# Kernel tuning notes

Hardware: AMD Instinct MI355X
Metric: run time of the kernel (lower is better)

## Reference

```python
import jax, jax.numpy as jnp
import numpy as np

RANK = 192      # wbits=4 -> rank 192 in prepare_grouped_lora
QMAX = 15.0     # 2**4 - 1 for 4-bit asymmetric quantization
EPS = 1e-8

def _fake_quant_weight(w):
    # Per-output-channel asymmetric min-max fake quantization (4-bit).
    wmin = jnp.minimum(w.min(axis=1, keepdims=True), 0.0)
    wmax = jnp.maximum(w.max(axis=1, keepdims=True), 0.0)
    scale = jnp.maximum((wmax - wmin) / QMAX, EPS)
    zero = jnp.round(-wmin / scale)
    q = jnp.clip(jnp.round(w / scale) + zero, 0.0, QMAX)
    return (q - zero) * scale

def setup_inputs() -> dict:
    key = jax.random.key(0)
    k1, k2, k3, k4, k5 = jax.random.split(key, 5)
    B, S, IN, OUT = 4, 2048, 4096, 11008
    x = jax.random.normal(k1, (B, S, IN), dtype=jnp.float32)
    weight = jax.random.normal(k2, (OUT, IN), dtype=jnp.float32) * 0.02
    Bd = jax.random.normal(k3, (OUT, RANK), dtype=jnp.float32) * 0.01
    Bu = jax.random.normal(k4, (RANK, IN), dtype=jnp.float32) * 0.01
    bias = jax.random.normal(k5, (OUT,), dtype=jnp.float32) * 0.01
    return {"x": x, "weight": weight, "Bd": Bd, "Bu": Bu, "bias": bias}

def reference(x, weight, Bd, Bu, bias):
    # LoRA delta: Bd[:, :rank] @ Bu[:rank, :]  (rank=192 for 4-bit)
    delta = jnp.einsum('or,ri->oi', Bd[:, :RANK], Bu[:RANK, :])
    w = _fake_quant_weight(weight + delta)          # [out, in]
    out = jnp.einsum('bsi,oi->bso', x, w) + bias    # F.linear
    return out
```

## Files before the change

kernel.cpp:

```cpp
#include <hip/hip_runtime.h>
#include <stdint.h>

#define M_ROWS 8192
#define N_OUT  11008
#define K_IN   4096
#define RANK   192

typedef __attribute__((ext_vector_type(8))) short bf16x8;
typedef __attribute__((ext_vector_type(4))) float f32x4;

#define GLDS16(g, l) __builtin_amdgcn_global_load_lds( \
    (const __attribute__((address_space(1))) unsigned int*)(g), \
    (__attribute__((address_space(3))) unsigned int*)(l), 16, 0, 0)

static __device__ __forceinline__ unsigned short f2bf(float f) {
    union { float f; unsigned int u; } a; a.f = f;
    unsigned int u = a.u;
    u += 0x7fffu + ((u >> 16) & 1u);
    return (unsigned short)(u >> 16);
}

__global__ __launch_bounds__(256) void k_delta_minmax(
    const float* __restrict__ Wg, const float* __restrict__ Bd,
    const float* __restrict__ Bu, float* __restrict__ wq,
    float* __restrict__ pmin, float* __restrict__ pmax)
{
    __shared__ float bdT[RANK][68];
    __shared__ float buS[8][256];
    const int t  = threadIdx.x;
    const int tx = t & 31, ty = t >> 5;
    const int row0 = blockIdx.x * 64;
    const int col0 = blockIdx.y * 256;

    for (int i = t; i < 64 * RANK; i += 256) {
        int r = i / RANK, k = i - r * RANK;
        bdT[k][r] = Bd[(size_t)(row0 + r) * RANK + k];
    }

    float acc[8][8];
#pragma unroll
    for (int a = 0; a < 8; ++a)
#pragma unroll
        for (int b = 0; b < 8; ++b) acc[a][b] = 0.0f;

    for (int kc = 0; kc < RANK / 8; ++kc) {
        __syncthreads();
#pragma unroll
        for (int j = 0; j < 8; ++j)
            buS[j][t] = Bu[(size_t)(kc * 8 + j) * K_IN + col0 + t];
        __syncthreads();
#pragma unroll
        for (int k = 0; k < 8; ++k) {
            float bd[8], bu[8];
#pragma unroll
            for (int rr = 0; rr < 8; ++rr) bd[rr] = bdT[kc * 8 + k][ty * 8 + rr];
#pragma unroll
            for (int cc = 0; cc < 8; ++cc) bu[cc] = buS[k][tx + 32 * cc];
#pragma unroll
            for (int rr = 0; rr < 8; ++rr)
#pragma unroll
                for (int cc = 0; cc < 8; ++cc)
                    acc[rr][cc] = fmaf(bd[rr], bu[cc], acc[rr][cc]);
        }
    }

    float rmin[8], rmax[8];
#pragma unroll
    for (int rr = 0; rr < 8; ++rr) { rmin[rr] = 3.0e38f; rmax[rr] = -3.0e38f; }
#pragma unroll
    for (int rr = 0; rr < 8; ++rr) {
        size_t gr = (size_t)(row0 + ty * 8 + rr);
#pragma unroll
        for (int cc = 0; cc < 8; ++cc) {
            size_t gc = (size_t)(col0 + tx + 32 * cc);
            float w = Wg[gr * K_IN + gc] + acc[rr][cc];
            wq[gr * K_IN + gc] = w;
            rmin[rr] = fminf(rmin[rr], w);
            rmax[rr] = fmaxf(rmax[rr], w);
        }
    }
#pragma unroll
    for (int off = 16; off >= 1; off >>= 1) {
#pragma unroll
        for (int rr = 0; rr < 8; ++rr) {
            rmin[rr] = fminf(rmin[rr], __shfl_xor(rmin[rr], off, 64));
            rmax[rr] = fmaxf(rmax[rr], __shfl_xor(rmax[rr], off, 64));
        }
    }
    if (tx == 0) {
#pragma unroll
        for (int rr = 0; rr < 8; ++rr) {
            int gr = row0 + ty * 8 + rr;
            pmin[(size_t)gr * 16 + blockIdx.y] = rmin[rr];
            pmax[(size_t)gr * 16 + blockIdx.y] = rmax[rr];
        }
    }
}

__global__ __launch_bounds__(256) void k_scale_zero(
    const float* __restrict__ pmin, const float* __restrict__ pmax,
    float* __restrict__ scale, float* __restrict__ zero)
{
    int r = blockIdx.x * 256 + threadIdx.x;
    if (r >= N_OUT) return;
    float mn = 0.0f, mx = 0.0f;
#pragma unroll
    for (int i = 0; i < 16; ++i) {
        mn = fminf(mn, pmin[(size_t)r * 16 + i]);
        mx = fmaxf(mx, pmax[(size_t)r * 16 + i]);
    }
    float s = fmaxf((mx - mn) / 15.0f, 1e-8f);
    scale[r] = s;
    zero[r] = rintf(-mn / s);
}

__global__ __launch_bounds__(256) void k_quant_cast(
    const float* __restrict__ wq, const float* __restrict__ scale,
    const float* __restrict__ zero, unsigned short* __restrict__ wb)
{
    size_t i = ((size_t)blockIdx.x * 256 + threadIdx.x) * 4;
    int r = (int)(i >> 12);
    float s = scale[r], z = zero[r];
    float4 v = *(const float4*)(wq + i);
    float in[4] = {v.x, v.y, v.z, v.w};
    unsigned short h[4];
#pragma unroll
    for (int j = 0; j < 4; ++j) {
        float q = rintf(in[j] / s) + z;
        q = fminf(fmaxf(q, 0.0f), 15.0f);
        h[j] = f2bf((q - z) * s);
    }
    unsigned int lo = (unsigned int)h[0] | ((unsigned int)h[1] << 16);
    unsigned int hi = (unsigned int)h[2] | ((unsigned int)h[3] << 16);
    *(unsigned long long*)(wb + i) = ((unsigned long long)hi << 32) | lo;
}

__global__ __launch_bounds__(256) void k_cast_x(
    const float* __restrict__ x, unsigned short* __restrict__ xb)
{
    size_t i = ((size_t)blockIdx.x * 256 + threadIdx.x) * 4;
    float4 v = *(const float4*)(x + i);
    unsigned int lo = (unsigned int)f2bf(v.x) | ((unsigned int)f2bf(v.y) << 16);
    unsigned int hi = (unsigned int)f2bf(v.z) | ((unsigned int)f2bf(v.w) << 16);
    *(unsigned long long*)(xb + i) = ((unsigned long long)hi << 32) | lo;
}

#define NT (K_IN / 64)

__global__ __launch_bounds__(512, 2) void k_gemm(
    const unsigned short* __restrict__ A,
    const unsigned short* __restrict__ W,
    const float* __restrict__ bias,
    float* __restrict__ C)
{
    extern __shared__ char lds[];

    const int tid  = threadIdx.x;
    const int lane = tid & 63;
    const int w    = tid >> 6;
    const int wr   = w >> 2;
    const int wn   = w & 3;

    const int orig = blockIdx.y * gridDim.x + blockIdx.x;
    const int swz  = (orig & 7) * 172 + (orig >> 3);
    const int bm0  = (swz & 31) << 8;
    const int bn0  = (swz >> 5) << 8;

    const int lrow = lane & 15, lq = lane >> 4;
    const int colA = (lq * 16) ^ (((lrow >> 3) & 1) << 5);

    const int srow = w * 16 + (lane >> 2);
    const int scol = ((lane & 3) * 8) ^ (((lane >> 5) & 1) * 16);

    const unsigned short* pa = A + (size_t)(bm0 + srow) * K_IN + scol;
    const unsigned short* pw = W + (size_t)(bn0 + srow) * K_IN + scol;
    char* ldsw = lds + w * 1024;

    char* abase = lds + (wr * 64 + lrow) * 64 + colA;
    char* bbase = lds + 32768 + (wn * 32 + lrow) * 64 + colA;

#define STAGE_A(D, KT, H) { \
    const unsigned short* s_ = pa + (size_t)((H) * 128) * K_IN + (KT) * 64; \
    char* l_ = ldsw + (D) * 65536 + (H) * 16384; \
    GLDS16(s_,      l_); \
    GLDS16(s_ + 32, l_ + 8192); }
#define STAGE_B(D, KT, H) { \
    const unsigned short* s_ = pw + (size_t)((H) * 128) * K_IN + (KT) * 64; \
    char* l_ = ldsw + (D) * 65536 + 32768 + (H) * 16384; \
    GLDS16(s_,      l_); \
    GLDS16(s_ + 32, l_ + 8192); }

#define READ_A(D, MH) { \
    _Pragma("unroll") for (int mi = 0; mi < 4; ++mi) { \
        af[mi][0] = *(const bf16x8*)(abase + (D) * 65536 + (MH) * 16384 + mi * 1024); \
        af[mi][1] = *(const bf16x8*)(abase + (D) * 65536 + (MH) * 16384 + 8192 + mi * 1024); } }
#define READ_B(D, NH, B_) { \
    _Pragma("unroll") for (int ni = 0; ni < 2; ++ni) { \
        B_[ni][0] = *(const bf16x8*)(bbase + (D) * 65536 + (NH) * 16384 + ni * 1024); \
        B_[ni][1] = *(const bf16x8*)(bbase + (D) * 65536 + (NH) * 16384 + 8192 + ni * 1024); } }

#define MFMA_Q(MH, NH, B_) { \
    __builtin_amdgcn_s_setprio(1); \
    _Pragma("unroll") for (int mi = 0; mi < 4; ++mi) \
    _Pragma("unroll") for (int ni = 0; ni < 2; ++ni) { \
        acc[MH][NH][mi][ni] = __builtin_amdgcn_mfma_f32_16x16x32_bf16( \
            af[mi][0], B_[ni][0], acc[MH][NH][mi][ni], 0, 0, 0); \
        acc[MH][NH][mi][ni] = __builtin_amdgcn_mfma_f32_16x16x32_bf16( \
            af[mi][1], B_[ni][1], acc[MH][NH][mi][ni], 0, 0, 0); } \
    __builtin_amdgcn_s_setprio(0); }

    f32x4 acc[2][2][4][2] = {};
    bf16x8 af[4][2], b0[2][2], b1[2][2];

    STAGE_A(0, 0, 0); STAGE_A(0, 0, 1); STAGE_B(0, 0, 0); STAGE_B(0, 0, 1);
    STAGE_A(1, 1, 0); STAGE_B(1, 1, 1); STAGE_A(1, 1, 1);
    asm volatile("s_waitcnt vmcnt(6)" ::: "memory");
    __builtin_amdgcn_s_barrier();

#define TILE_BODY(T, D, DN) { \
     \
    READ_A(D, 0); READ_B(D, 0, b0); \
    if ((T) + 1 < NT) STAGE_B(DN, (T) + 1, 0); \
    __builtin_amdgcn_s_barrier(); \
    MFMA_Q(0, 0, b0); \
    __builtin_amdgcn_s_barrier(); \
     \
    READ_B(D, 1, b1); \
    if ((T) + 2 < NT) STAGE_A(D, (T) + 2, 0); \
    __builtin_amdgcn_s_barrier(); \
    MFMA_Q(0, 1, b1); \
    __builtin_amdgcn_s_barrier(); \
     \
    READ_A(D, 1); \
    if ((T) + 2 < NT) STAGE_B(D, (T) + 2, 1); \
    __builtin_amdgcn_s_barrier(); \
    MFMA_Q(1, 1, b1); \
    __builtin_amdgcn_s_barrier(); \
     \
    if ((T) + 2 < NT) { \
        STAGE_A(D, (T) + 2, 1); \
        asm volatile("s_waitcnt vmcnt(6)" ::: "memory"); \
    } else { \
        asm volatile("s_waitcnt vmcnt(0)" ::: "memory"); \
    } \
    __builtin_amdgcn_s_barrier(); \
    MFMA_Q(1, 0, b0); \
    __builtin_amdgcn_s_barrier(); }

#pragma unroll 1
    for (int tt = 0; tt < NT; tt += 2) {
        TILE_BODY(tt,     0, 1);
        TILE_BODY(tt + 1, 1, 0);
    }

#pragma unroll
    for (int mh = 0; mh < 2; ++mh)
#pragma unroll
    for (int mi = 0; mi < 4; ++mi) {
        const int row = bm0 + mh * 128 + wr * 64 + mi * 16 + lq * 4;
#pragma unroll
        for (int nh = 0; nh < 2; ++nh)
#pragma unroll
        for (int ni = 0; ni < 2; ++ni) {
            const int col = bn0 + nh * 128 + wn * 32 + ni * 16 + lrow;
            const float bb = bias[col];
            const f32x4 v = acc[mh][nh][mi][ni];
#pragma unroll
            for (int r = 0; r < 4; ++r)
                C[(size_t)(row + r) * N_OUT + col] = v[r] + bb;
        }
    }
}

extern "C" void kernel_launch(void* const* d_in, const int* in_sizes, int n_in,
                              void* d_out, int out_size, void* d_ws, size_t ws_size,
                              hipStream_t stream)
{
    const float* x      = (const float*)d_in[0];
    const float* weight = (const float*)d_in[1];
    const float* Bd     = (const float*)d_in[2];
    const float* Bu     = (const float*)d_in[3];
    const float* bias   = (const float*)d_in[4];
    float* out = (float*)d_out;

    char* ws = (char*)d_ws;
    float*          wq    = (float*)(ws);
    float*          pmin  = (float*)(ws + 180355072);
    float*          pmax  = (float*)(ws + 181059584);
    float*          scale = (float*)(ws + 181764096);
    float*          zero  = (float*)(ws + 181808128);
    unsigned short* wb    = (unsigned short*)(ws + 181852160);
    unsigned short* xb    = (unsigned short*)(ws + 272029696);

    static bool attr_set = false;
    if (!attr_set) {
        hipFuncSetAttribute((const void*)k_gemm,
                            hipFuncAttributeMaxDynamicSharedMemorySize, 131072);
        attr_set = true;
    }

    k_delta_minmax<<<dim3(N_OUT / 64, K_IN / 256), 256, 0, stream>>>(
        weight, Bd, Bu, wq, pmin, pmax);
    k_scale_zero<<<(N_OUT + 255) / 256, 256, 0, stream>>>(pmin, pmax, scale, zero);
    k_quant_cast<<<(N_OUT * (K_IN / 4)) / 256, 256, 0, stream>>>(wq, scale, zero, wb);
    k_cast_x<<<(M_ROWS * (K_IN / 4)) / 256, 256, 0, stream>>>(x, xb);
    k_gemm<<<dim3(M_ROWS / 256, N_OUT / 256), 512, 131072, stream>>>(xb, wb, bias, out);
}
```

Baseline: 1.708 ms.

## Software-pipeline LDS fragment reads with fine-grained waitcnts; vectorize delta kernel

Restructures the GEMM main loop so LDS fragment reads for the next quadrant or tile are issued ahead of the current MFMA block. It double-buffers A and B fragments in registers and replaces full barriers before each MFMA block with explicit vmcnt/lgkmcnt waits. The last two tiles are peeled so the wait counts match the loads actually outstanding. The LoRA delta kernel also drops its Bu LDS staging in favour of direct float4 global loads and writes W with float4 stores. The aim is to hide LDS and global latency behind MFMA work, at the cost of more registers and hand-tuned wait counts that must stay correct.

```diff
diff --git a/kernel.cpp b/kernel.cpp
--- a/kernel.cpp
+++ b/kernel.cpp
@@ -12,6 +12,10 @@
 #define GLDS16(g, l) __builtin_amdgcn_global_load_lds( \
     (const __attribute__((address_space(1))) unsigned int*)(g), \
     (__attribute__((address_space(3))) unsigned int*)(l), 16, 0, 0)
+
+#define STR_IMPL(x) #x
+#define VMW(n) asm volatile("s_waitcnt vmcnt(" STR_IMPL(n) ")" ::: "memory")
+#define LKW(n) asm volatile("s_waitcnt lgkmcnt(" STR_IMPL(n) ")" ::: "memory")
 
 static __device__ __forceinline__ unsigned short f2bf(float f) {
     union { float f; unsigned int u; } a; a.f = f;
@@ -26,7 +30,6 @@
     float* __restrict__ pmin, float* __restrict__ pmax)
 {
     __shared__ float bdT[RANK][68];
-    __shared__ float buS[8][256];
     const int t  = threadIdx.x;
     const int tx = t & 31, ty = t >> 5;
     const int row0 = blockIdx.x * 64;
@@ -36,6 +39,7 @@
         int r = i / RANK, k = i - r * RANK;
         bdT[k][r] = Bd[(size_t)(row0 + r) * RANK + k];
     }
+    __syncthreads();
 
     float acc[8][8];
 #pragma unroll
@@ -43,25 +47,21 @@
 #pragma unroll
         for (int b = 0; b < 8; ++b) acc[a][b] = 0.0f;
 
-    for (int kc = 0; kc < RANK / 8; ++kc) {
-        __syncthreads();
-#pragma unroll
-        for (int j = 0; j < 8; ++j)
-            buS[j][t] = Bu[(size_t)(kc * 8 + j) * K_IN + col0 + t];
-        __syncthreads();
-#pragma unroll
-        for (int k = 0; k < 8; ++k) {
-            float bd[8], bu[8];
-#pragma unroll
-            for (int rr = 0; rr < 8; ++rr) bd[rr] = bdT[kc * 8 + k][ty * 8 + rr];
-#pragma unroll
-            for (int cc = 0; cc < 8; ++cc) bu[cc] = buS[k][tx + 32 * cc];
-#pragma unroll
-            for (int rr = 0; rr < 8; ++rr)
-#pragma unroll
-                for (int cc = 0; cc < 8; ++cc)
-                    acc[rr][cc] = fmaf(bd[rr], bu[cc], acc[rr][cc]);
-        }
+    const float* bup = Bu + col0 + tx * 8;
+#pragma unroll 2
+    for (int k = 0; k < RANK; ++k) {
+        const float4 b0 = *(const float4*)(bup);
+        const float4 b1 = *(const float4*)(bup + 4);
+        bup += K_IN;
+        const float4 d0 = *(const float4*)&bdT[k][ty * 8];
+        const float4 d1 = *(const float4*)&bdT[k][ty * 8 + 4];
+        const float bd[8] = {d0.x, d0.y, d0.z, d0.w, d1.x, d1.y, d1.z, d1.w};
+        const float bv[8] = {b0.x, b0.y, b0.z, b0.w, b1.x, b1.y, b1.z, b1.w};
+#pragma unroll
+        for (int rr = 0; rr < 8; ++rr)
+#pragma unroll
+            for (int cc = 0; cc < 8; ++cc)
+                acc[rr][cc] = fmaf(bd[rr], bv[cc], acc[rr][cc]);
     }
 
     float rmin[8], rmax[8];
@@ -69,15 +69,22 @@
     for (int rr = 0; rr < 8; ++rr) { rmin[rr] = 3.0e38f; rmax[rr] = -3.0e38f; }
 #pragma unroll
     for (int rr = 0; rr < 8; ++rr) {
-        size_t gr = (size_t)(row0 + ty * 8 + rr);
+        const size_t gr = (size_t)(row0 + ty * 8 + rr);
+        const float* wrow = Wg + gr * K_IN + col0 + tx * 8;
+        const float4 w0 = *(const float4*)(wrow);
+        const float4 w1 = *(const float4*)(wrow + 4);
+        const float wv[8] = {w0.x, w0.y, w0.z, w0.w, w1.x, w1.y, w1.z, w1.w};
+        float o[8];
 #pragma unroll
         for (int cc = 0; cc < 8; ++cc) {
-            size_t gc = (size_t)(col0 + tx + 32 * cc);
-            float w = Wg[gr * K_IN + gc] + acc[rr][cc];
-            wq[gr * K_IN + gc] = w;
+            float w = wv[cc] + acc[rr][cc];
+            o[cc] = w;
             rmin[rr] = fminf(rmin[rr], w);
             rmax[rr] = fmaxf(rmax[rr], w);
         }
+        float* orow = wq + gr * K_IN + col0 + tx * 8;
+        *(float4*)(orow)     = make_float4(o[0], o[1], o[2], o[3]);
+        *(float4*)(orow + 4) = make_float4(o[4], o[5], o[6], o[7]);
     }
 #pragma unroll
     for (int off = 16; off >= 1; off >>= 1) {
@@ -190,68 +197,74 @@
     GLDS16(s_,      l_); \
     GLDS16(s_ + 32, l_ + 8192); }
 
-#define READ_A(D, MH) { \
+#define READ_A(AF, D, MH) { \
     _Pragma("unroll") for (int mi = 0; mi < 4; ++mi) { \
-        af[mi][0] = *(const bf16x8*)(abase + (D) * 65536 + (MH) * 16384 + mi * 1024); \
-        af[mi][1] = *(const bf16x8*)(abase + (D) * 65536 + (MH) * 16384 + 8192 + mi * 1024); } }
-#define READ_B(D, NH, B_) { \
+        AF[mi][0] = *(const bf16x8*)(abase + (D) * 65536 + (MH) * 16384 + mi * 1024); \
+        AF[mi][1] = *(const bf16x8*)(abase + (D) * 65536 + (MH) * 16384 + 8192 + mi * 1024); } }
+#define READ_B(B_, D, NH) { \
     _Pragma("unroll") for (int ni = 0; ni < 2; ++ni) { \
         B_[ni][0] = *(const bf16x8*)(bbase + (D) * 65536 + (NH) * 16384 + ni * 1024); \
         B_[ni][1] = *(const bf16x8*)(bbase + (D) * 65536 + (NH) * 16384 + 8192 + ni * 1024); } }
 
-#define MFMA_Q(MH, NH, B_) { \
+#define MFMA_Q(MH, NH, AF, B_) { \
     __builtin_amdgcn_s_setprio(1); \
     _Pragma("unroll") for (int mi = 0; mi < 4; ++mi) \
     _Pragma("unroll") for (int ni = 0; ni < 2; ++ni) { \
         acc[MH][NH][mi][ni] = __builtin_amdgcn_mfma_f32_16x16x32_bf16( \
-            af[mi][0], B_[ni][0], acc[MH][NH][mi][ni], 0, 0, 0); \
+            AF[mi][0], B_[ni][0], acc[MH][NH][mi][ni], 0, 0, 0); \
         acc[MH][NH][mi][ni] = __builtin_amdgcn_mfma_f32_16x16x32_bf16( \
-            af[mi][1], B_[ni][1], acc[MH][NH][mi][ni], 0, 0, 0); } \
+            AF[mi][1], B_[ni][1], acc[MH][NH][mi][ni], 0, 0, 0); } \
     __builtin_amdgcn_s_setprio(0); }
 
     f32x4 acc[2][2][4][2] = {};
-    bf16x8 af[4][2], b0[2][2], b1[2][2];
-
-    STAGE_A(0, 0, 0); STAGE_A(0, 0, 1); STAGE_B(0, 0, 0); STAGE_B(0, 0, 1);
-    STAGE_A(1, 1, 0); STAGE_B(1, 1, 1); STAGE_A(1, 1, 1);
-    asm volatile("s_waitcnt vmcnt(6)" ::: "memory");
+    bf16x8 af0[4][2], af1[4][2], bE[2][2], bO[2][2];
+
+    STAGE_A(0, 0, 0); STAGE_B(0, 0, 0); STAGE_B(0, 0, 1); STAGE_A(0, 0, 1);
+    STAGE_A(1, 1, 0); STAGE_B(1, 1, 0); STAGE_B(1, 1, 1); STAGE_A(1, 1, 1);
+    VMW(10);
     __builtin_amdgcn_s_barrier();
-
-#define TILE_BODY(T, D, DN) { \
+    READ_A(af0, 0, 0);
+    READ_B(bE, 0, 0);
+    LKW(0);
+    __builtin_amdgcn_s_barrier();
+
+#define TILE_BODY(T, D, DN, BH0, BH1, STG, RDN, V0, V1, V2, V3, LK2, LK3) { \
      \
-    READ_A(D, 0); READ_B(D, 0, b0); \
-    if ((T) + 1 < NT) STAGE_B(DN, (T) + 1, 0); \
-    __builtin_amdgcn_s_barrier(); \
-    MFMA_Q(0, 0, b0); \
+    READ_B(BH1, D, 1); \
+    LKW(4); \
+    if (STG) STAGE_A(D, (T) + 2, 0); \
+    VMW(V0); \
+    MFMA_Q(0, 0, af0, BH0); \
     __builtin_amdgcn_s_barrier(); \
      \
-    READ_B(D, 1, b1); \
-    if ((T) + 2 < NT) STAGE_A(D, (T) + 2, 0); \
-    __builtin_amdgcn_s_barrier(); \
-    MFMA_Q(0, 1, b1); \
+    READ_A(af1, D, 1); \
+    LKW(8); \
+    if (STG) STAGE_B(D, (T) + 2, 0); \
+    VMW(V1); \
+    MFMA_Q(0, 1, af0, BH1); \
     __builtin_amdgcn_s_barrier(); \
      \
-    READ_A(D, 1); \
-    if ((T) + 2 < NT) STAGE_B(D, (T) + 2, 1); \
-    __builtin_amdgcn_s_barrier(); \
-    MFMA_Q(1, 1, b1); \
+    if (RDN) READ_A(af0, DN, 0); \
+    LKW(LK2); \
+    if (STG) STAGE_B(D, (T) + 2, 1); \
+    VMW(V2); \
+    MFMA_Q(1, 1, af1, BH1); \
     __builtin_amdgcn_s_barrier(); \
      \
-    if ((T) + 2 < NT) { \
-        STAGE_A(D, (T) + 2, 1); \
-        asm volatile("s_waitcnt vmcnt(6)" ::: "memory"); \
-    } else { \
-        asm volatile("s_waitcnt vmcnt(0)" ::: "memory"); \
-    } \
-    __builtin_amdgcn_s_barrier(); \
-    MFMA_Q(1, 0, b0); \
+    if (RDN) READ_B(BH1, DN, 0); \
+    LKW(LK3); \
+    if (STG) STAGE_A(D, (T) + 2, 1); \
+    VMW(V3); \
+    MFMA_Q(1, 0, af1, BH0); \
     __builtin_amdgcn_s_barrier(); }
 
 #pragma unroll 1
-    for (int tt = 0; tt < NT; tt += 2) {
-        TILE_BODY(tt,     0, 1);
-        TILE_BODY(tt + 1, 1, 0);
-    }
+    for (int tt = 0; tt < NT - 2; tt += 2) {
+        TILE_BODY(tt,     0, 1, bE, bO, 1, 1, 10, 10, 10, 10, 8, 4);
+        TILE_BODY(tt + 1, 1, 0, bO, bE, 1, 1, 10, 10, 10, 10, 8, 4);
+    }
+    TILE_BODY(NT - 2, 0, 1, bE, bO, 0, 1, 8, 6, 4, 2, 8, 4);
+    TILE_BODY(NT - 1, 1, 0, bO, bE, 0, 0, 0, 0, 0, 0, 0, 0);
 
 #pragma unroll
     for (int mh = 0; mh < 2; ++mh)
```

Result: slower. 1.807 ms (+5.8%).
